# Performance work log

Hardware: AMD Instinct MI355X
Metric: run time of the kernel (lower is better)

Reference implementation:

```python
import jax, jax.numpy as jnp
import numpy as np
import math

B, T, C = 4, 2048, 1024
H = 16  # parallelAttentionPathways
D = C // H  # head dim = 64


def setup_inputs() -> dict:
    key = jax.random.key(0)
    k1, k2, k3 = jax.random.split(key, 3)
    x = jax.random.normal(k1, (B, T, C), dtype=jnp.float32)
    w_qkv = jax.random.normal(k2, (3 * C, C), dtype=jnp.float32) * (1.0 / math.sqrt(C))
    w_out = jax.random.normal(k3, (C, C), dtype=jnp.float32) * (1.0 / math.sqrt(C))
    return {"x": x, "w_qkv": w_qkv, "w_out": w_out}


def reference(x, w_qkv, w_out):
    b, t, c = x.shape
    # qkv projection: torch Linear y = x @ W^T (no bias)
    qkv = jnp.einsum('btc,fc->btf', x, w_qkv)  # [B,T,3C]
    q, k, v = jnp.split(qkv, 3, axis=-1)
    # [B,H,T,D]
    q = q.reshape(b, t, H, D).transpose(0, 2, 1, 3)
    k = k.reshape(b, t, H, D).transpose(0, 2, 1, 3)
    v = v.reshape(b, t, H, D).transpose(0, 2, 1, 3)
    scale = 1.0 / math.sqrt(D)
    att = jnp.einsum('bhqd,bhkd->bhqk', q, k) * scale  # [B,H,T,T]
    causal = jnp.tril(jnp.ones((t, t), dtype=bool))
    att = jnp.where(causal[None, None], att, -jnp.inf)
    att = jax.nn.softmax(att, axis=-1)
    # dropoutRate=0.0 -> dropout is identity (eval-mode determinism)
    y = jnp.einsum('bhqk,bhkd->bhqd', att, v)  # [B,H,T,D]
    y = y.transpose(0, 2, 1, 3).reshape(b, t, c)
    return jnp.einsum('btc,fc->btf', y, w_out)
```

## Files before the change

### kernel.cpp

```cpp
#include <hip/hip_runtime.h>
#include <hip/hip_bf16.h>
#include <stdint.h>


using bf16 = __hip_bfloat16;
typedef __attribute__((ext_vector_type(8))) __bf16 bf16x8;
typedef __attribute__((ext_vector_type(8))) unsigned short u16x8;
typedef __attribute__((ext_vector_type(4))) unsigned short u16x4;
typedef __attribute__((ext_vector_type(4))) float f32x4;
typedef unsigned short ushort_t;

#define MFMA16(a, b, c) __builtin_amdgcn_mfma_f32_16x16x32_bf16((a), (b), (c), 0, 0, 0)

__device__ __forceinline__ bf16x8 ld_frag(const ushort_t* p) {
  const u16x8 u = *(const u16x8*)p;
  return __builtin_bit_cast(bf16x8, u);
}

__device__ __forceinline__ ushort_t f2bf(float f) {
  return __builtin_bit_cast(ushort_t, __float2bfloat16(f));
}

__device__ __forceinline__ void gl2lds16(const void* g, void* lds) {
  __builtin_amdgcn_global_load_lds((const __attribute__((address_space(1))) void*)g,
                                   (__attribute__((address_space(3))) void*)lds,
                                   16, 0, 0);
}

__global__ void detect_dtype(const ushort_t* __restrict__ x, int* __restrict__ flag) {
  __shared__ int red[256];
  const int tid = threadIdx.x;
  int cnt = 0;
  for (int i = tid; i < 4096; i += 256) {
    const int e = (x[i] & 0x7FFF) >> 7;
    cnt += (e >= 117 && e <= 133) ? 1 : 0;
  }
  red[tid] = cnt;
  __syncthreads();
  for (int s = 128; s > 0; s >>= 1) {
    if (tid < s) red[tid] += red[tid + s];
    __syncthreads();
  }
  if (tid == 0) *flag = (red[0] < 3072) ? 1 : 0;
}

__global__ void cvt_to_bf16(const void* __restrict__ in, ushort_t* __restrict__ out,
                            int n, const int* __restrict__ flag) {
  const int i = (blockIdx.x * 256 + threadIdx.x) * 8;
  if (i >= n) return;
  if (*flag) {
    const float* p = (const float*)in + i;
    const float4 f0 = *(const float4*)p;
    const float4 f1 = *(const float4*)(p + 4);
    u16x8 u;
    u[0] = f2bf(f0.x); u[1] = f2bf(f0.y); u[2] = f2bf(f0.z); u[3] = f2bf(f0.w);
    u[4] = f2bf(f1.x); u[5] = f2bf(f1.y); u[6] = f2bf(f1.z); u[7] = f2bf(f1.w);
    *(u16x8*)(out + i) = u;
  } else {
    *(u16x8*)(out + i) = *(const u16x8*)((const ushort_t*)in + i);
  }
}

template <int EPI>
__global__ __launch_bounds__(256, 2)
void gemm_nt(const ushort_t* __restrict__ A, const void* __restrict__ Bw,
             const int* __restrict__ flag, int bExt,
             float* __restrict__ C0, ushort_t* __restrict__ Qo,
             ushort_t* __restrict__ Ko, ushort_t* __restrict__ Vt,
             int M, int N, int Kd) {
  __shared__ ushort_t sA[2][128 * 32];
  __shared__ ushort_t sB[2][128 * 32];
  const int tid = threadIdx.x;
  const int wave = tid >> 6, lane = tid & 63;
  const int quad = lane >> 4, l16 = lane & 15;
  const int wm = wave >> 1, wn = wave & 1;
  const long m0 = (long)blockIdx.y * 128;
  const long n0 = (long)blockIdx.x * 128;
  const int bF = bExt ? *flag : 0;

  f32x4 acc[4][4];
#pragma unroll
  for (int i = 0; i < 4; ++i)
#pragma unroll
    for (int j = 0; j < 4; ++j) acc[i][j] = (f32x4){0.f, 0.f, 0.f, 0.f};

  const int nt = Kd >> 5;

  auto stageA = [&](int buf, int k0) {
#pragma unroll
    for (int j = 0; j < 2; ++j) {
      const int chunk = wave * 2 + j;
      const int idx = chunk * 64 + lane;
      const int r = idx >> 2, c = idx & 3;
      gl2lds16(A + (m0 + r) * (long)Kd + k0 + c * 8,
               (char*)&sA[buf][0] + chunk * 1024);
    }
  };
  auto stageB = [&](int buf, int k0) {
    if (!bF) {
#pragma unroll
      for (int j = 0; j < 2; ++j) {
        const int chunk = wave * 2 + j;
        const int idx = chunk * 64 + lane;
        const int r = idx >> 2, c = idx & 3;
        gl2lds16((const ushort_t*)Bw + (n0 + r) * (long)Kd + k0 + c * 8,
                 (char*)&sB[buf][0] + chunk * 1024);
      }
    } else {
#pragma unroll
      for (int t2 = 0; t2 < 2; ++t2) {
        const int idx = t2 * 256 + tid;
        const int r = idx >> 2, c = idx & 3;
        const float* p = (const float*)Bw + (n0 + r) * (long)Kd + k0 + c * 8;
        const float4 f0 = *(const float4*)p;
        const float4 f1 = *(const float4*)(p + 4);
        u16x8 u;
        u[0] = f2bf(f0.x); u[1] = f2bf(f0.y); u[2] = f2bf(f0.z); u[3] = f2bf(f0.w);
        u[4] = f2bf(f1.x); u[5] = f2bf(f1.y); u[6] = f2bf(f1.z); u[7] = f2bf(f1.w);
        *(u16x8*)&sB[buf][r * 32 + c * 8] = u;
      }
    }
  };

  stageA(0, 0);
  stageB(0, 0);
  asm volatile("s_waitcnt vmcnt(0) lgkmcnt(0)" ::: "memory");
  __builtin_amdgcn_s_barrier();

  int cur = 0;
  for (int t = 0; t < nt; ++t) {
    if (t + 1 < nt) {
      const int k0n = (t + 1) << 5;
      stageA(cur ^ 1, k0n);
      stageB(cur ^ 1, k0n);
    }
    const ushort_t* cA = &sA[cur][0];
    const ushort_t* cB = &sB[cur][0];
    bf16x8 af[4], bfr[4];
#pragma unroll
    for (int i = 0; i < 4; ++i) {
      const int r = wm * 64 + i * 16 + l16;
      af[i] = ld_frag(&cA[r * 32 + quad * 8]);
    }
#pragma unroll
    for (int i = 0; i < 4; ++i) {
      const int r = wn * 64 + i * 16 + l16;
      bfr[i] = ld_frag(&cB[r * 32 + quad * 8]);
    }
#pragma unroll
    for (int i = 0; i < 4; ++i)
#pragma unroll
      for (int j = 0; j < 4; ++j) acc[i][j] = MFMA16(af[i], bfr[j], acc[i][j]);
    asm volatile("s_waitcnt vmcnt(0) lgkmcnt(0)" ::: "memory");
    __builtin_amdgcn_s_barrier();
    cur ^= 1;
  }

#pragma unroll
  for (int i = 0; i < 4; ++i) {
#pragma unroll
    for (int j = 0; j < 4; ++j) {
      if (EPI == 0) {
#pragma unroll
        for (int reg = 0; reg < 4; ++reg) {
          const long m = m0 + wm * 64 + i * 16 + quad * 4 + reg;
          const long n = n0 + wn * 64 + j * 16 + l16;
          C0[m * N + n] = acc[i][j][reg];
        }
      } else {
        const long n = n0 + wn * 64 + j * 16 + l16;
        const int which = (int)(n >> 10);
        const int h = (int)((n >> 6) & 15);
        const int d = (int)(n & 63);
        const long mbase = m0 + wm * 64 + i * 16 + quad * 4;
        const long b = mbase >> 11;
        const long tb = mbase & 2047;
        if (which == 2) {
          u16x4 pk;
#pragma unroll
          for (int reg = 0; reg < 4; ++reg) pk[reg] = f2bf(acc[i][j][reg]);
          *(u16x4*)&Vt[((b * 16 + h) * 64 + d) * 2048 + tb] = pk;
        } else {
          ushort_t* dst = (which == 0) ? Qo : Ko;
#pragma unroll
          for (int reg = 0; reg < 4; ++reg)
            dst[((b * 16 + h) * 2048 + tb + reg) * 64 + d] = f2bf(acc[i][j][reg]);
        }
      }
    }
  }
}


__device__ __forceinline__ void softmax_tile(f32x4* s, int kb, int qg, bool need_mask,
                                             float& m_i, float& l_i, f32x4* oacc) {
  float rmax = -1e30f;
  if (need_mask) {
#pragma unroll
    for (int nt = 0; nt < 4; ++nt) {
#pragma unroll
      for (int reg = 0; reg < 4; ++reg) {
        float v = s[nt][reg];
        if (kb + nt * 16 + reg > qg) v = -1e30f;
        s[nt][reg] = v;
        rmax = fmaxf(rmax, v);
      }
    }
  } else {
#pragma unroll
    for (int nt = 0; nt < 4; ++nt) {
#pragma unroll
      for (int reg = 0; reg < 4; ++reg) rmax = fmaxf(rmax, s[nt][reg]);
    }
  }
  rmax = fmaxf(rmax, __shfl_xor(rmax, 16, 64));
  rmax = fmaxf(rmax, __shfl_xor(rmax, 32, 64));
  float mnew = fmaxf(m_i, rmax);
  if (__all(rmax - m_i <= 5.5f)) {
    mnew = m_i;
  } else {
    const float alpha = __expf(m_i - mnew);
    l_i *= alpha;
#pragma unroll
    for (int dt = 0; dt < 4; ++dt) oacc[dt] *= alpha;
    m_i = mnew;
  }
  float rs = 0.f;
#pragma unroll
  for (int nt = 0; nt < 4; ++nt) {
#pragma unroll
    for (int reg = 0; reg < 4; ++reg) {
      const float p = __expf(s[nt][reg] - mnew);
      s[nt][reg] = p;
      rs += p;
    }
  }
  rs += __shfl_xor(rs, 16, 64);
  rs += __shfl_xor(rs, 32, 64);
  l_i += rs;
}

__device__ __forceinline__ void attn_job(const bf16x8 qf[2], const ushort_t* sKc,
                                         const ushort_t* sVc, ushort_t* sPw,
                                         int kv, int qg, bool need_mask,
                                         int quad, int l8, int l16,
                                         float& m_i, float& l_i, f32x4* oacc) {
  const f32x4 ZERO4 = {0.f, 0.f, 0.f, 0.f};
  const int off0 = ((quad ^ l8) << 3);
  const int off1 = (((quad + 4) ^ l8) << 3);
  f32x4 s[4];
#pragma unroll
  for (int nt = 0; nt < 4; ++nt) {
    const ushort_t* krow = sKc + (nt * 16 + l16) * 64;
    s[nt] = MFMA16(ld_frag(krow + off0), qf[0], ZERO4);
    s[nt] = MFMA16(ld_frag(krow + off1), qf[1], s[nt]);
  }
  softmax_tile(s, kv * 64 + quad * 4, qg, need_mask, m_i, l_i, oacc);

  asm volatile("s_waitcnt lgkmcnt(0)" ::: "memory");
#pragma unroll
  for (int nt = 0; nt < 4; ++nt) {
    u16x4 pk;
#pragma unroll
    for (int reg = 0; reg < 4; ++reg) pk[reg] = f2bf(s[nt][reg]);
    *(u16x4*)&sPw[l16 * 64 + (((4 * nt + quad) << 2) ^ (l8 << 3))] = pk;
  }
  asm volatile("s_waitcnt lgkmcnt(0)" ::: "memory");
  bf16x8 pf0 = ld_frag(&sPw[l16 * 64 + off0]);
  bf16x8 pf1 = ld_frag(&sPw[l16 * 64 + off1]);
#pragma unroll
  for (int dt = 0; dt < 4; ++dt) {
    const ushort_t* vrow = sVc + (dt * 16 + l16) * 64;
    oacc[dt] = MFMA16(ld_frag(vrow + off0), pf0, oacc[dt]);
    oacc[dt] = MFMA16(ld_frag(vrow + off1), pf1, oacc[dt]);
  }
}

__global__ __launch_bounds__(256, 4)
void attn_causal(const ushort_t* __restrict__ Qg, const ushort_t* __restrict__ Kg,
                 const ushort_t* __restrict__ Vt, ushort_t* __restrict__ Yg) {
  __shared__ ushort_t sK[2][64 * 64];
  __shared__ ushort_t sV[2][64 * 64];
  __shared__ ushort_t sP[64 * 64];
  const int tid = threadIdx.x;
  const int wave = tid >> 6, lane = tid & 63;
  const int quad = lane >> 4, l16 = lane & 15, l8 = lane & 7;
  const f32x4 ZERO4 = {0.f, 0.f, 0.f, 0.f};
  const int lin = blockIdx.y * 16 + blockIdx.x;
  const int logical = (lin & 7) * 128 + (lin >> 3);
  const int qx = logical & 15, bh = logical >> 4;
  const int qtA = qx, qtB = 31 - qx;
  const size_t base = (size_t)bh * 2048 * 64;
  ushort_t* sPw = sP + wave * 16 * 64;

  const int srow = lane >> 3;
  const int scol = ((lane & 7) ^ srow) << 3;

  bf16x8 qfA[2], qfB[2];
#pragma unroll
  for (int tile = 0; tile < 2; ++tile) {
    const int qt = tile ? qtB : qtA;
    const size_t qrow = base + (size_t)(qt * 64 + wave * 16 + l16) * 64;
#pragma unroll
    for (int kk = 0; kk < 2; ++kk) {
      const u16x8 u = *(const u16x8*)(Qg + qrow + (kk * 4 + quad) * 8);
      u16x8 w;
#pragma unroll
      for (int e = 0; e < 8; ++e)
        w[e] = f2bf(__bfloat162float(__builtin_bit_cast(bf16, (ushort_t)u[e])) * 0.125f);
      const bf16x8 f = __builtin_bit_cast(bf16x8, w);
      if (tile) qfB[kk] = f; else qfA[kk] = f;
    }
  }

  float mA = -1e30f, lA = 0.f, mB = -1e30f, lB = 0.f;
  f32x4 oA[4], oB[4];
#pragma unroll
  for (int dt = 0; dt < 4; ++dt) {
    oA[dt] = ZERO4;
    oB[dt] = ZERO4;
  }
  const int qgA = qtA * 64 + wave * 16 + l16;
  const int qgB = qtB * 64 + wave * 16 + l16;
  const int qmA = qtA * 64 + wave * 16;
  const int qmB = qtB * 64 + wave * 16;

#pragma unroll
  for (int j = 0; j < 2; ++j) {
    const int chunk = wave * 2 + j;
    gl2lds16(Kg + base + (size_t)(chunk * 8 + srow) * 64 + scol,
             (char*)&sK[0][0] + chunk * 1024);
    gl2lds16(Vt + base + (size_t)(chunk * 8 + srow) * 2048 + scol,
             (char*)&sV[0][0] + chunk * 1024);
  }

  for (int kv = 0; kv <= qtB; ++kv) {
    const int cur = kv & 1;
    __syncthreads();
    if (kv < qtB) {
      const int kn = kv + 1;
#pragma unroll
      for (int j = 0; j < 2; ++j) {
        const int chunk = wave * 2 + j;
        gl2lds16(Kg + base + (size_t)(kn * 64 + chunk * 8 + srow) * 64 + scol,
                 (char*)&sK[cur ^ 1][0] + chunk * 1024);
        gl2lds16(Vt + base + (size_t)(chunk * 8 + srow) * 2048 + kn * 64 + scol,
                 (char*)&sV[cur ^ 1][0] + chunk * 1024);
      }
    }
    const ushort_t* sKc = &sK[cur][0];
    const ushort_t* sVc = &sV[cur][0];
    attn_job(qfB, sKc, sVc, sPw, kv, qgB, kv * 64 + 63 > qmB, quad, l8, l16, mB, lB, oB);
    if (kv <= qtA)
      attn_job(qfA, sKc, sVc, sPw, kv, qgA, kv * 64 + 63 > qmA, quad, l8, l16, mA, lA, oA);
  }

  const int b = bh >> 4, h = bh & 15;
#pragma unroll
  for (int tile = 0; tile < 2; ++tile) {
    const int qt = tile ? qtB : qtA;
    const float linv = 1.f / (tile ? lB : lA);
    const f32x4* o = tile ? oB : oA;
    const int t = qt * 64 + wave * 16 + l16;
#pragma unroll
    for (int dt = 0; dt < 4; ++dt) {
      u16x4 pk;
#pragma unroll
      for (int reg = 0; reg < 4; ++reg) pk[reg] = f2bf(o[dt][reg] * linv);
      *(u16x4*)&Yg[(((size_t)b * 2048 + t) * 16 + h) * 64 + dt * 16 + quad * 4] = pk;
    }
  }
}

extern "C" void kernel_launch(void* const* d_in, const int* in_sizes, int n_in,
                              void* d_out, int out_size, void* d_ws, size_t ws_size,
                              hipStream_t stream) {
  const void* x = d_in[0];
  const void* w_qkv = d_in[1];
  const void* w_out = d_in[2];
  float* out = (float*)d_out;

  const size_t per = (size_t)4 * 16 * 2048 * 64;
  const size_t nwqkv = (size_t)3072 * 1024;
  const size_t nwout = (size_t)1024 * 1024;
  ushort_t* qws = (ushort_t*)d_ws;
  ushort_t* kws = qws + per;
  ushort_t* vTws = kws + per;
  ushort_t* xyws = vTws + per;
  ushort_t* wqkvb = xyws + per;
  ushort_t* woutb = wqkvb + nwqkv;
  int* flag = (int*)(woutb + nwout);
  const size_t need = (size_t)(4 * per + nwqkv + nwout) * 2 + 16;
  const bool pre = ws_size >= need;
  (void)in_sizes; (void)n_in; (void)out_size;

  dim3 blk(256);
  if (!pre) flag = (int*)(xyws + per);
  detect_dtype<<<1, 256, 0, stream>>>((const ushort_t*)x, flag);
  cvt_to_bf16<<<4096, 256, 0, stream>>>(x, xyws, (int)per, flag);
  if (pre) {
    cvt_to_bf16<<<1536, 256, 0, stream>>>(w_qkv, wqkvb, (int)nwqkv, flag);
    cvt_to_bf16<<<512, 256, 0, stream>>>(w_out, woutb, (int)nwout, flag);
    gemm_nt<1><<<dim3(24, 64), blk, 0, stream>>>(xyws, wqkvb, flag, 0, nullptr,
                                                 qws, kws, vTws, 8192, 3072, 1024);
    attn_causal<<<dim3(16, 64), blk, 0, stream>>>(qws, kws, vTws, xyws);
    gemm_nt<0><<<dim3(8, 64), blk, 0, stream>>>(xyws, woutb, flag, 0, out,
                                                nullptr, nullptr, nullptr,
                                                8192, 1024, 1024);
  } else {
    gemm_nt<1><<<dim3(24, 64), blk, 0, stream>>>(xyws, w_qkv, flag, 1, nullptr,
                                                 qws, kws, vTws, 8192, 3072, 1024);
    attn_causal<<<dim3(16, 64), blk, 0, stream>>>(qws, kws, vTws, xyws);
    gemm_nt<0><<<dim3(8, 64), blk, 0, stream>>>(xyws, w_out, flag, 1, out,
                                                nullptr, nullptr, nullptr,
                                                8192, 1024, 1024);
  }
}
```

Before: 265.4 us.

## Triple-buffer GEMM LDS staging and merge conversion kernels into one launch

The GEMM moves from double to triple-buffered LDS with prefetch distance two. It waits with a partial vmcnt so the next tile's global-to-LDS loads can stay in flight during compute, and it drops the trailing barrier per k-step. The three fp32-to-bf16 conversion launches are merged into one cvt_all kernel to cut launch overhead. The cost is 50% more LDS per block, which may reduce occupancy. The vmcnt(4) count depends on how many loads stageA and stageB issue, so a wrong count could create a race.

```diff
diff --git a/kernel.cpp b/kernel.cpp
--- a/kernel.cpp
+++ b/kernel.cpp
@@ -44,20 +44,31 @@
   if (tid == 0) *flag = (red[0] < 3072) ? 1 : 0;
 }
 
-__global__ void cvt_to_bf16(const void* __restrict__ in, ushort_t* __restrict__ out,
-                            int n, const int* __restrict__ flag) {
-  const int i = (blockIdx.x * 256 + threadIdx.x) * 8;
-  if (i >= n) return;
+__global__ void cvt_all(const void* __restrict__ x, const void* __restrict__ wq,
+                        const void* __restrict__ wo, ushort_t* __restrict__ xo,
+                        ushort_t* __restrict__ wqo, ushort_t* __restrict__ woo,
+                        const int* __restrict__ flag) {
+  const int b = blockIdx.x;
+  const void* src;
+  ushort_t* dst;
+  int i;
+  if (b < 4096) {
+    src = x; dst = xo; i = b * 2048 + threadIdx.x * 8;
+  } else if (b < 5632) {
+    src = wq; dst = wqo; i = (b - 4096) * 2048 + threadIdx.x * 8;
+  } else {
+    src = wo; dst = woo; i = (b - 5632) * 2048 + threadIdx.x * 8;
+  }
   if (*flag) {
-    const float* p = (const float*)in + i;
+    const float* p = (const float*)src + i;
     const float4 f0 = *(const float4*)p;
     const float4 f1 = *(const float4*)(p + 4);
     u16x8 u;
     u[0] = f2bf(f0.x); u[1] = f2bf(f0.y); u[2] = f2bf(f0.z); u[3] = f2bf(f0.w);
     u[4] = f2bf(f1.x); u[5] = f2bf(f1.y); u[6] = f2bf(f1.z); u[7] = f2bf(f1.w);
-    *(u16x8*)(out + i) = u;
+    *(u16x8*)(dst + i) = u;
   } else {
-    *(u16x8*)(out + i) = *(const u16x8*)((const ushort_t*)in + i);
+    *(u16x8*)(dst + i) = *(const u16x8*)((const ushort_t*)src + i);
   }
 }
 
@@ -68,8 +79,8 @@
              float* __restrict__ C0, ushort_t* __restrict__ Qo,
              ushort_t* __restrict__ Ko, ushort_t* __restrict__ Vt,
              int M, int N, int Kd) {
-  __shared__ ushort_t sA[2][128 * 32];
-  __shared__ ushort_t sB[2][128 * 32];
+  __shared__ ushort_t sA[3][128 * 32];
+  __shared__ ushort_t sB[3][128 * 32];
   const int tid = threadIdx.x;
   const int wave = tid >> 6, lane = tid & 63;
   const int quad = lane >> 4, l16 = lane & 15;
@@ -124,18 +135,23 @@
 
   stageA(0, 0);
   stageB(0, 0);
-  asm volatile("s_waitcnt vmcnt(0) lgkmcnt(0)" ::: "memory");
-  __builtin_amdgcn_s_barrier();
-
-  int cur = 0;
+  if (nt > 1) {
+    stageA(1, 32);
+    stageB(1, 32);
+  }
+
   for (int t = 0; t < nt; ++t) {
-    if (t + 1 < nt) {
-      const int k0n = (t + 1) << 5;
-      stageA(cur ^ 1, k0n);
-      stageB(cur ^ 1, k0n);
-    }
-    const ushort_t* cA = &sA[cur][0];
-    const ushort_t* cB = &sB[cur][0];
+    if (!bF && t + 1 < nt) {
+      asm volatile("s_waitcnt vmcnt(4) lgkmcnt(0)\n\ts_barrier" ::: "memory");
+    } else {
+      asm volatile("s_waitcnt vmcnt(0) lgkmcnt(0)\n\ts_barrier" ::: "memory");
+    }
+    if (t + 2 < nt) {
+      stageA((t + 2) % 3, (t + 2) << 5);
+      stageB((t + 2) % 3, (t + 2) << 5);
+    }
+    const ushort_t* cA = &sA[t % 3][0];
+    const ushort_t* cB = &sB[t % 3][0];
     bf16x8 af[4], bfr[4];
 #pragma unroll
     for (int i = 0; i < 4; ++i) {
@@ -151,9 +167,6 @@
     for (int i = 0; i < 4; ++i)
 #pragma unroll
       for (int j = 0; j < 4; ++j) acc[i][j] = MFMA16(af[i], bfr[j], acc[i][j]);
-    asm volatile("s_waitcnt vmcnt(0) lgkmcnt(0)" ::: "memory");
-    __builtin_amdgcn_s_barrier();
-    cur ^= 1;
   }
 
 #pragma unroll
@@ -397,10 +410,8 @@
   dim3 blk(256);
   if (!pre) flag = (int*)(xyws + per);
   detect_dtype<<<1, 256, 0, stream>>>((const ushort_t*)x, flag);
-  cvt_to_bf16<<<4096, 256, 0, stream>>>(x, xyws, (int)per, flag);
   if (pre) {
-    cvt_to_bf16<<<1536, 256, 0, stream>>>(w_qkv, wqkvb, (int)nwqkv, flag);
-    cvt_to_bf16<<<512, 256, 0, stream>>>(w_out, woutb, (int)nwout, flag);
+    cvt_all<<<6144, 256, 0, stream>>>(x, w_qkv, w_out, xyws, wqkvb, woutb, flag);
     gemm_nt<1><<<dim3(24, 64), blk, 0, stream>>>(xyws, wqkvb, flag, 0, nullptr,
                                                  qws, kws, vTws, 8192, 3072, 1024);
     attn_causal<<<dim3(16, 64), blk, 0, stream>>>(qws, kws, vTws, xyws);
@@ -408,6 +419,7 @@
                                                 nullptr, nullptr, nullptr,
                                                 8192, 1024, 1024);
   } else {
+    cvt_all<<<4096, 256, 0, stream>>>(x, nullptr, nullptr, xyws, nullptr, nullptr, flag);
     gemm_nt<1><<<dim3(24, 64), blk, 0, stream>>>(xyws, w_qkv, flag, 1, nullptr,
                                                  qws, kws, vTws, 8192, 3072, 1024);
     attn_causal<<<dim3(16, 64), blk, 0, stream>>>(qws, kws, vTws, xyws);
```

New measurement: 262.1 us. No clear change (-1.2%).
